# Kernel optimization log

Measured on AMD Instinct MI355X. Metric: run time of the kernel, lower is better.

## Reference

```python
import jax, jax.numpy as jnp
import numpy as np

B, S, D, H = 8, 1024, 768, 12
HD = D // H  # head_dim = 64


def setup_inputs() -> dict:
    key = jax.random.key(0)
    ks = jax.random.split(key, 9)
    s = 0.02
    return {
        "hidden_states": jax.random.normal(ks[0], (B, S, D), dtype=jnp.float32),
        "Wq": jax.random.normal(ks[1], (D, D), dtype=jnp.float32) * s,
        "bq": jnp.zeros((D,), dtype=jnp.float32),
        "Wk": jax.random.normal(ks[2], (D, D), dtype=jnp.float32) * s,
        "bk": jnp.zeros((D,), dtype=jnp.float32),
        "Wv": jax.random.normal(ks[3], (D, D), dtype=jnp.float32) * s,
        "bv": jnp.zeros((D,), dtype=jnp.float32),
        "Wo": jax.random.normal(ks[4], (D, D), dtype=jnp.float32) * s,
        "bo": jnp.zeros((D,), dtype=jnp.float32),
    }


def reference(hidden_states, Wq, bq, Wk, bk, Wv, bv, Wo, bo):
    b, s, d = hidden_states.shape
    scale = 1.0 / jnp.sqrt(jnp.asarray(HD, dtype=hidden_states.dtype))
    # projections (weights stored as [in, out])
    q = hidden_states @ Wq + bq
    k = hidden_states @ Wk + bk
    v = hidden_states @ Wv + bv
    # [B, H, S, HD]
    q = q.reshape(b, s, H, HD).transpose(0, 2, 1, 3)
    k = k.reshape(b, s, H, HD).transpose(0, 2, 1, 3)
    v = v.reshape(b, s, H, HD).transpose(0, 2, 1, 3)
    # explicit O(S^2) attention, matching the original unfused math
    attn = jnp.einsum("bhqd,bhkd->bhqk", q, k) * scale
    attn = jax.nn.softmax(attn, axis=-1)
    out = jnp.einsum("bhqk,bhkd->bhqd", attn, v)
    out = out.transpose(0, 2, 1, 3).reshape(b, s, d)
    return out @ Wo + bo
```

## Files before the change

kernel.cpp:

```cpp
#include <hip/hip_runtime.h>
#include <stdint.h>

#define DEV __device__ __forceinline__

typedef __attribute__((ext_vector_type(8))) short bf16x8;
typedef __attribute__((ext_vector_type(4))) float f32x4;

#define MFMA16(a,b,c) __builtin_amdgcn_mfma_f32_16x16x32_bf16((a),(b),(c),0,0,0)

#define GL_LDS(SRC, DST) \
  __builtin_amdgcn_global_load_lds( \
      (const __attribute__((address_space(1))) void*)(SRC), \
      (__attribute__((address_space(3))) void*)(DST), 16, 0, 0)

DEV unsigned short f2bf(float x){
  union { float f; unsigned u; } v; v.f = x;
  unsigned r = v.u + 0x7fffu + ((v.u >> 16) & 1u);
  return (unsigned short)(r >> 16);
}
DEV unsigned pack2(float a, float b){
  return (unsigned)f2bf(a) | ((unsigned)f2bf(b) << 16);
}
DEV bf16x8 mk_bf16x8(unsigned w0, unsigned w1, unsigned w2, unsigned w3){
  union { uint4 u; bf16x8 v; } cv;
  cv.u = make_uint4(w0, w1, w2, w3);
  return cv.v;
}
DEV void bar(){
  asm volatile("" ::: "memory");
  __builtin_amdgcn_s_barrier();
  asm volatile("" ::: "memory");
}

__global__ void cast_x_kernel(const float* __restrict__ x, uint4* __restrict__ out){
  int i = blockIdx.x * 256 + threadIdx.x;
  const float4* p = (const float4*)x + (size_t)i * 2;
  float4 a = p[0], b = p[1];
  out[i] = make_uint4(pack2(a.x,a.y), pack2(a.z,a.w), pack2(b.x,b.y), pack2(b.z,b.w));
}

__global__ void trans_w_kernel(const float* __restrict__ W0, const float* __restrict__ W1,
                               const float* __restrict__ W2, const float* __restrict__ W3,
                               unsigned short* __restrict__ T0, unsigned short* __restrict__ T1,
                               unsigned short* __restrict__ T2, unsigned short* __restrict__ T3){
  const float* W; unsigned short* T;
  switch (blockIdx.z) {
    case 0:  W = W0; T = T0; break;
    case 1:  W = W1; T = T1; break;
    case 2:  W = W2; T = T2; break;
    default: W = W3; T = T3; break;
  }
  __shared__ float tile[32][33];
  const int i0 = blockIdx.y * 32, o0 = blockIdx.x * 32;
  const int t = threadIdx.x;
  const int ir = t >> 3, oc = (t & 7) * 4;
  float4 v = *(const float4*)(W + (size_t)(i0 + ir) * 768 + o0 + oc);
  tile[ir][oc+0] = v.x; tile[ir][oc+1] = v.y; tile[ir][oc+2] = v.z; tile[ir][oc+3] = v.w;
  __syncthreads();
  const int orow = t >> 3, ic = (t & 7) * 4;
  uint2 w;
  w.x = pack2(tile[ic+0][orow], tile[ic+1][orow]);
  w.y = pack2(tile[ic+2][orow], tile[ic+3][orow]);
  *(uint2*)(T + (size_t)(o0 + orow) * 768 + i0 + ic) = w;
}

__launch_bounds__(512, 2)
__global__ void gemm_qkv(const unsigned short* __restrict__ Wcat,
                         const unsigned short* __restrict__ X16,
                         const float* __restrict__ bq, const float* __restrict__ bk,
                         const float* __restrict__ bv,
                         unsigned short* __restrict__ Qb, unsigned short* __restrict__ Kb,
                         unsigned short* __restrict__ VTb)
{
  __shared__ __align__(16) unsigned char a_lds[2][2][18432];
  __shared__ __align__(16) unsigned char b_lds[2][2][16384];
  const int tid = threadIdx.x;
  const int lane = tid & 63;
  const int wid = tid >> 6;
  const int lin = blockIdx.x;
  const int nid = (lin & 7) * 32 + (lin >> 3);
  const int m0 = (nid & 7) * 288;
  const int n0 = (nid >> 3) * 256;
  const int wm = wid >> 2, wn = wid & 3;

  const int c1 = tid,               r1 = ((c1 >> 6) << 4) + (c1 & 15), kg1 = (c1 >> 4) & 3;
  const int c2 = 512 + tid,         r2 = ((c2 >> 6) << 4) + (c2 & 15), kg2 = (c2 >> 4) & 3;
  const int c3 = 1024 + (tid & 127),r3 = ((c3 >> 6) << 4) + (c3 & 15), kg3 = (c3 >> 4) & 3;
  const unsigned short* Abase = Wcat + (size_t)m0 * 768;
  const unsigned short* Bbase = X16  + (size_t)n0 * 768;

  #define STAGE_A(TILE, KK) do {                                                   \
    const int ko_ = (TILE) * 64 + (KK) * 32;                                       \
    GL_LDS(Abase + (size_t)r1 * 768 + ko_ + kg1 * 8, &a_lds[(TILE)&1][KK][c1*16]); \
    GL_LDS(Abase + (size_t)r2 * 768 + ko_ + kg2 * 8, &a_lds[(TILE)&1][KK][c2*16]); \
    GL_LDS(Abase + (size_t)r3 * 768 + ko_ + kg3 * 8, &a_lds[(TILE)&1][KK][c3*16]); \
  } while (0)
  #define STAGE_B(TILE, KK) do {                                                   \
    const int ko_ = (TILE) * 64 + (KK) * 32;                                       \
    GL_LDS(Bbase + (size_t)r1 * 768 + ko_ + kg1 * 8, &b_lds[(TILE)&1][KK][c1*16]); \
    GL_LDS(Bbase + (size_t)r2 * 768 + ko_ + kg2 * 8, &b_lds[(TILE)&1][KK][c2*16]); \
  } while (0)

  #define PHASE(BUF, KK, NH, STAGE_STMT)                                           \
  {                                                                                \
    bf16x8 bfr0 = *(const bf16x8*)&b_lds[BUF][KK][((wn*4+(NH)*2+0)*64+lane)*16];   \
    bf16x8 bfr1 = *(const bf16x8*)&b_lds[BUF][KK][((wn*4+(NH)*2+1)*64+lane)*16];   \
    STAGE_STMT;                                                                    \
    bar();                                                                         \
    __builtin_amdgcn_s_setprio(1);                                                 \
    _Pragma("unroll")                                                              \
    for (int mb = 0; mb < 9; ++mb) {                                               \
      bf16x8 af = *(const bf16x8*)&a_lds[BUF][KK][((wm*9+mb)*64+lane)*16];         \
      acc[mb][(NH)*2+0] = MFMA16(af, bfr0, acc[mb][(NH)*2+0]);                     \
      acc[mb][(NH)*2+1] = MFMA16(af, bfr1, acc[mb][(NH)*2+1]);                     \
    }                                                                              \
    __builtin_amdgcn_s_setprio(0);                                                 \
    asm volatile("s_waitcnt vmcnt(10)" ::: "memory");                              \
    bar();                                                                         \
  }

  f32x4 acc[9][4] = {};

  STAGE_A(0, 0);
  STAGE_B(0, 0);
  STAGE_A(0, 1);
  STAGE_B(0, 1);
  STAGE_A(1, 0);
  STAGE_B(1, 0);
  asm volatile("s_waitcnt vmcnt(10)" ::: "memory");
  bar();

  for (int i = 0; i < 6; ++i) {
    const int k0t = 2 * i, k1t = 2 * i + 1;
    const bool pf = (i < 5);
    PHASE(0, 0, 0, { STAGE_A(k1t, 1); })
    PHASE(0, 0, 1, { STAGE_B(k1t, 1); })
    PHASE(0, 1, 0, { if (pf) STAGE_A(k0t + 2, 0); })
    PHASE(0, 1, 1, { if (pf) STAGE_B(k0t + 2, 0); })
    PHASE(1, 0, 0, { if (pf) STAGE_A(k0t + 2, 1); })
    PHASE(1, 0, 1, { if (pf) STAGE_B(k0t + 2, 1); })
    PHASE(1, 1, 0, { if (pf) STAGE_A(k1t + 2, 0); })
    PHASE(1, 1, 1, { if (pf) STAGE_B(k1t + 2, 0); })
  }
  #undef PHASE
  #undef STAGE_A
  #undef STAGE_B

  const int l15 = lane & 15, lg = lane >> 4;
  #pragma unroll
  for (int mb = 0; mb < 9; ++mb) {
    const int chan_g = m0 + wm * 144 + mb * 16 + lg * 4;
    const int sel  = chan_g / 768;
    const int chan = chan_g - sel * 768;
    const int h = chan >> 6, hd = chan & 63;
    #pragma unroll
    for (int nb = 0; nb < 4; ++nb) {
      const int coll = wn * 64 + nb * 16 + l15;
      const int sg   = n0 + coll;
      const int b = sg >> 10, s = sg & 1023;
      f32x4 a = acc[mb][nb];
      if (sel != 2) {
        float4 bi = *(const float4*)((sel == 0 ? bq : bk) + chan);
        uint2 w;
        w.x = pack2(a[0] + bi.x, a[1] + bi.y);
        w.y = pack2(a[2] + bi.z, a[3] + bi.w);
        unsigned short* o = (sel == 0 ? Qb : Kb);
        *(uint2*)(o + ((size_t)(b * 12 + h) * 1024 + s) * 64 + hd) = w;
      } else {
        float4 bi = *(const float4*)(bv + chan);
        size_t base = ((size_t)(b * 12 + h) * 64 + hd) * 1024 + s;
        VTb[base       ] = f2bf(a[0] + bi.x);
        VTb[base + 1024] = f2bf(a[1] + bi.y);
        VTb[base + 2048] = f2bf(a[2] + bi.z);
        VTb[base + 3072] = f2bf(a[3] + bi.w);
      }
    }
  }
}

__launch_bounds__(256, 3)
__global__ void gemm_out(const unsigned short* __restrict__ matA,
                         const unsigned short* __restrict__ matB,
                         float* __restrict__ outp,
                         const float* __restrict__ bias)
{
  __shared__ __align__(16) unsigned char ldsA[2][4096];
  __shared__ __align__(16) unsigned char ldsB[2][8192];
  const int lane = threadIdx.x & 63, wid = threadIdx.x >> 6;
  const int lin = blockIdx.x;
  const int nid = (lin & 7) * 96 + (lin >> 3);
  const int m0 = (nid % 12) * 64;
  const int n0 = (nid / 12) * 128;
  const int wm = wid >> 1, wn = wid & 1;

  f32x4 acc[2][4] = {};

  for (int t = 0; t < 24; ++t) {
    const int buf = t & 1;
    const int k0 = t * 32;
    {
      const int c   = wid * 64 + lane;
      const int row = ((c >> 6) << 4) + (c & 15);
      const int kk  = ((c >> 4) & 3) * 8;
      const unsigned short* sa = matA + (size_t)(m0 + row) * 768 + k0 + kk;
      GL_LDS(sa, &ldsA[buf][c * 16]);
    }
    #pragma unroll
    for (int i = 0; i < 2; ++i) {
      const int c   = i * 256 + wid * 64 + lane;
      const int row = ((c >> 6) << 4) + (c & 15);
      const int kk  = ((c >> 4) & 3) * 8;
      const unsigned short* sb = matB + (size_t)(n0 + row) * 768 + k0 + kk;
      GL_LDS(sb, &ldsB[buf][c * 16]);
    }
    __syncthreads();

    bf16x8 afr[2], bfr[4];
    #pragma unroll
    for (int mb = 0; mb < 2; ++mb)
      afr[mb] = *(const bf16x8*)&ldsA[buf][((wm * 2 + mb) * 64 + lane) * 16];
    #pragma unroll
    for (int nb = 0; nb < 4; ++nb)
      bfr[nb] = *(const bf16x8*)&ldsB[buf][((wn * 4 + nb) * 64 + lane) * 16];
    #pragma unroll
    for (int mb = 0; mb < 2; ++mb)
      #pragma unroll
      for (int nb = 0; nb < 4; ++nb)
        acc[mb][nb] = MFMA16(afr[mb], bfr[nb], acc[mb][nb]);
  }

  const int l15 = lane & 15, lg = lane >> 4;
  #pragma unroll
  for (int mb = 0; mb < 2; ++mb) {
    #pragma unroll
    for (int nb = 0; nb < 4; ++nb) {
      const int rowl = wm * 32 + mb * 16 + lg * 4;
      const int coll = wn * 64 + nb * 16 + l15;
      f32x4 a = acc[mb][nb];
      int chan = m0 + rowl, sg = n0 + coll;
      float4 bi = *(const float4*)(bias + chan);
      float4 o = make_float4(a[0] + bi.x, a[1] + bi.y, a[2] + bi.z, a[3] + bi.w);
      *(float4*)(outp + (size_t)sg * 768 + chan) = o;
    }
  }
}

__launch_bounds__(256, 4)
__global__ void attn_kernel(const unsigned short* __restrict__ Q,
                            const unsigned short* __restrict__ K,
                            const unsigned short* __restrict__ VT,
                            unsigned short* __restrict__ AO)
{
  __shared__ __align__(16) unsigned char kbuf[8192];
  __shared__ __align__(16) unsigned char vbuf[8192];
  const int lane = threadIdx.x & 63, wid = threadIdx.x >> 6;
  const int l15 = lane & 15, lg = lane >> 4;
  const int bh = blockIdx.x;
  const int q0 = blockIdx.y * 128 + wid * 32;
  const unsigned short* Qp = Q  + (size_t)bh * 65536;
  const unsigned short* Kp = K  + (size_t)bh * 65536;
  const unsigned short* Vp = VT + (size_t)bh * 65536;

  bf16x8 qf[2][2];
  #pragma unroll
  for (int f = 0; f < 2; ++f)
    #pragma unroll
    for (int kc = 0; kc < 2; ++kc)
      qf[f][kc] = *(const bf16x8*)(Qp + (size_t)(q0 + f * 16 + l15) * 64 + kc * 32 + lg * 8);

  f32x4 acco[2][4] = {};
  float lsum[2] = {0.f, 0.f};

  const int src0 = l15 + ((lg & 1) << 5);
  const int src1 = src0 + 16;
  const bool hi = (lg & 2) != 0;

  for (int t = 0; t < 16; ++t) {
    const int kv0 = t * 64;
    #pragma unroll
    for (int i = 0; i < 2; ++i) {
      const int g = wid * 2 + i;
      const unsigned short* sk = Kp + (size_t)(kv0 + (g >> 1) * 16 + l15) * 64 + (g & 1) * 32 + lg * 8;
      GL_LDS(sk, &kbuf[g * 1024]);
      const unsigned short* sv = Vp + (size_t)((g >> 1) * 16 + l15) * 1024 + kv0 + (g & 1) * 32 + lg * 8;
      GL_LDS(sv, &vbuf[g * 1024]);
    }
    __syncthreads();

    f32x4 sc[2][4] = {};
    #pragma unroll
    for (int mb = 0; mb < 4; ++mb) {
      #pragma unroll
      for (int kc = 0; kc < 2; ++kc) {
        bf16x8 kf = *(const bf16x8*)&kbuf[((mb * 2 + kc) * 64 + lane) * 16];
        sc[0][mb] = MFMA16(kf, qf[0][kc], sc[0][mb]);
        sc[1][mb] = MFMA16(kf, qf[1][kc], sc[1][mb]);
      }
    }
    unsigned p01[2][4], p23[2][4];
    #pragma unroll
    for (int f = 0; f < 2; ++f) {
      float sum = 0.f;
      #pragma unroll
      for (int mb = 0; mb < 4; ++mb) {
        float e0 = __expf(sc[f][mb][0] * 0.125f);
        float e1 = __expf(sc[f][mb][1] * 0.125f);
        float e2 = __expf(sc[f][mb][2] * 0.125f);
        float e3 = __expf(sc[f][mb][3] * 0.125f);
        sum += (e0 + e1) + (e2 + e3);
        p01[f][mb] = pack2(e0, e1);
        p23[f][mb] = pack2(e2, e3);
      }
      sum += __shfl_xor(sum, 16);
      sum += __shfl_xor(sum, 32);
      lsum[f] += sum;
    }
    bf16x8 pf[2][2];
    #pragma unroll
    for (int f = 0; f < 2; ++f) {
      #pragma unroll
      for (int c = 0; c < 2; ++c) {
        unsigned a0 = __shfl(p01[f][2*c], src0), b0 = __shfl(p01[f][2*c+1], src0);
        unsigned a1 = __shfl(p23[f][2*c], src0), b1 = __shfl(p23[f][2*c+1], src0);
        unsigned a2 = __shfl(p01[f][2*c], src1), b2 = __shfl(p01[f][2*c+1], src1);
        unsigned a3 = __shfl(p23[f][2*c], src1), b3 = __shfl(p23[f][2*c+1], src1);
        pf[f][c] = mk_bf16x8(hi ? b0 : a0, hi ? b1 : a1, hi ? b2 : a2, hi ? b3 : a3);
      }
    }
    #pragma unroll
    for (int hb = 0; hb < 4; ++hb) {
      #pragma unroll
      for (int c = 0; c < 2; ++c) {
        bf16x8 vf = *(const bf16x8*)&vbuf[((hb * 2 + c) * 64 + lane) * 16];
        acco[0][hb] = MFMA16(vf, pf[0][c], acco[0][hb]);
        acco[1][hb] = MFMA16(vf, pf[1][c], acco[1][hb]);
      }
    }
    __syncthreads();
  }

  const int b = bh / 12, h = bh % 12;
  #pragma unroll
  for (int f = 0; f < 2; ++f) {
    const float rl = 1.0f / lsum[f];
    const int s = q0 + f * 16 + l15;
    const size_t base = ((size_t)(b * 1024 + s)) * 768 + h * 64;
    #pragma unroll
    for (int hb = 0; hb < 4; ++hb) {
      uint2 w;
      w.x = pack2(acco[f][hb][0] * rl, acco[f][hb][1] * rl);
      w.y = pack2(acco[f][hb][2] * rl, acco[f][hb][3] * rl);
      *(uint2*)(AO + base + hb * 16 + lg * 4) = w;
    }
  }
}

extern "C" void kernel_launch(void* const* d_in, const int* in_sizes, int n_in,
                              void* d_out, int out_size, void* d_ws, size_t ws_size,
                              hipStream_t stream)
{
  const float* hs = (const float*)d_in[0];
  const float* Wq = (const float*)d_in[1];
  const float* bq = (const float*)d_in[2];
  const float* Wk = (const float*)d_in[3];
  const float* bk = (const float*)d_in[4];
  const float* Wv = (const float*)d_in[5];
  const float* bv = (const float*)d_in[6];
  const float* Wo = (const float*)d_in[7];
  const float* bo = (const float*)d_in[8];

  const size_t SZ_X = (size_t)8192 * 768 * 2;
  const size_t SZ_W = (size_t)768 * 768 * 2;
  const size_t NEED = SZ_X * 5 + SZ_W * 4;
  if (ws_size < NEED) return;

  char* ws = (char*)d_ws;
  unsigned short* X16 = (unsigned short*)ws;
  unsigned short* Wqt = (unsigned short*)(ws + SZ_X);
  unsigned short* Wkt = Wqt + 768 * 768;
  unsigned short* Wvt = Wkt + 768 * 768;
  unsigned short* Wot = Wvt + 768 * 768;
  unsigned short* Qb  = (unsigned short*)(ws + SZ_X + 4 * SZ_W);
  unsigned short* Kb  = Qb  + (size_t)8192 * 768;
  unsigned short* VTb = Kb  + (size_t)8192 * 768;
  unsigned short* AOb = VTb + (size_t)8192 * 768;

  cast_x_kernel<<<dim3(3072), dim3(256), 0, stream>>>(hs, (uint4*)X16);
  trans_w_kernel<<<dim3(24, 24, 4), dim3(256), 0, stream>>>(Wq, Wk, Wv, Wo, Wqt, Wkt, Wvt, Wot);

  gemm_qkv<<<dim3(256), dim3(512), 0, stream>>>(Wqt, X16, bq, bk, bv, Qb, Kb, VTb);

  attn_kernel<<<dim3(96, 8), dim3(256), 0, stream>>>(Qb, Kb, VTb, AOb);

  gemm_out<<<dim3(768), dim3(256), 0, stream>>>(Wot, AOb, (float*)d_out, bo);
}
```

Before: 148.6 us.

## Double-buffer K/V tiles in attention with async prefetch of next tile

```diff
diff --git a/kernel.cpp b/kernel.cpp
--- a/kernel.cpp
+++ b/kernel.cpp
@@ -251,8 +251,8 @@
                             const unsigned short* __restrict__ VT,
                             unsigned short* __restrict__ AO)
 {
-  __shared__ __align__(16) unsigned char kbuf[8192];
-  __shared__ __align__(16) unsigned char vbuf[8192];
+  __shared__ __align__(16) unsigned char kbuf[2][8192];
+  __shared__ __align__(16) unsigned char vbuf[2][8192];
   const int lane = threadIdx.x & 63, wid = threadIdx.x >> 6;
   const int l15 = lane & 15, lg = lane >> 4;
   const int bh = blockIdx.x;
@@ -275,24 +275,38 @@
   const int src1 = src0 + 16;
   const bool hi = (lg & 2) != 0;
 
+  #define ATTN_STAGE(TT) do {                                                        \
+    const int kv0s = (TT) * 64;                                                      \
+    _Pragma("unroll")                                                                \
+    for (int i = 0; i < 2; ++i) {                                                    \
+      const int g = wid * 2 + i;                                                     \
+      const unsigned short* sk = Kp + (size_t)(kv0s + (g >> 1) * 16 + l15) * 64      \
+                                    + (g & 1) * 32 + lg * 8;                         \
+      GL_LDS(sk, &kbuf[(TT) & 1][g * 1024]);                                         \
+      const unsigned short* sv = Vp + (size_t)((g >> 1) * 16 + l15) * 1024 + kv0s    \
+                                    + (g & 1) * 32 + lg * 8;                         \
+      GL_LDS(sv, &vbuf[(TT) & 1][g * 1024]);                                         \
+    }                                                                                \
+  } while (0)
+
+  ATTN_STAGE(0);
+
   for (int t = 0; t < 16; ++t) {
-    const int kv0 = t * 64;
-    #pragma unroll
-    for (int i = 0; i < 2; ++i) {
-      const int g = wid * 2 + i;
-      const unsigned short* sk = Kp + (size_t)(kv0 + (g >> 1) * 16 + l15) * 64 + (g & 1) * 32 + lg * 8;
-      GL_LDS(sk, &kbuf[g * 1024]);
-      const unsigned short* sv = Vp + (size_t)((g >> 1) * 16 + l15) * 1024 + kv0 + (g & 1) * 32 + lg * 8;
-      GL_LDS(sv, &vbuf[g * 1024]);
-    }
-    __syncthreads();
+    const int buf = t & 1;
+    if (t < 15) {
+      ATTN_STAGE(t + 1);
+      asm volatile("s_waitcnt vmcnt(4)" ::: "memory");
+    } else {
+      asm volatile("s_waitcnt vmcnt(0)" ::: "memory");
+    }
+    bar();
 
     f32x4 sc[2][4] = {};
     #pragma unroll
     for (int mb = 0; mb < 4; ++mb) {
       #pragma unroll
       for (int kc = 0; kc < 2; ++kc) {
-        bf16x8 kf = *(const bf16x8*)&kbuf[((mb * 2 + kc) * 64 + lane) * 16];
+        bf16x8 kf = *(const bf16x8*)&kbuf[buf][((mb * 2 + kc) * 64 + lane) * 16];
         sc[0][mb] = MFMA16(kf, qf[0][kc], sc[0][mb]);
         sc[1][mb] = MFMA16(kf, qf[1][kc], sc[1][mb]);
       }
@@ -331,13 +345,14 @@
     for (int hb = 0; hb < 4; ++hb) {
       #pragma unroll
       for (int c = 0; c < 2; ++c) {
-        bf16x8 vf = *(const bf16x8*)&vbuf[((hb * 2 + c) * 64 + lane) * 16];
+        bf16x8 vf = *(const bf16x8*)&vbuf[buf][((hb * 2 + c) * 64 + lane) * 16];
         acco[0][hb] = MFMA16(vf, pf[0][c], acco[0][hb]);
         acco[1][hb] = MFMA16(vf, pf[1][c], acco[1][hb]);
       }
     }
-    __syncthreads();
-  }
+    bar();
+  }
+  #undef ATTN_STAGE
 
   const int b = bh / 12, h = bh % 12;
   #pragma unroll
```

Result: no change. 148.5 us (-0.1%).
